# Kernel optimization log

Measured on AMD Instinct MI355X. Metric: run time of the kernel, lower is better.

The kernel has to match this reference:

```python
import jax, jax.numpy as jnp
import numpy as np

N_NODES = 100000
N_EDGES = 1600000
IN_DIM = 128
OUT_DIM = 64


def setup_inputs() -> dict:
    key = jax.random.key(0)
    k1, k2, k3, k4, k5 = jax.random.split(key, 5)
    return {
        "h_init": jax.random.normal(k1, (N_NODES, IN_DIM), dtype=jnp.float32),
        "W1": jax.random.normal(k2, (OUT_DIM, IN_DIM), dtype=jnp.float32),
        "a": jax.random.normal(k3, (1, OUT_DIM), dtype=jnp.float32),
        "src": jax.random.randint(k4, (N_EDGES,), 0, N_NODES, dtype=jnp.int64)
        if jax.config.jax_enable_x64 else jax.random.randint(k4, (N_EDGES,), 0, N_NODES, dtype=jnp.int32),
        "dst": jax.random.randint(k5, (N_EDGES,), 0, N_NODES, dtype=jnp.int32),
    }


def reference(h_init, W1, a, src, dst):
    N = h_init.shape[0]
    # node projection: [N, out_dim]
    h = h_init @ W1.T
    # per-edge diff feature: dst minus src (DGL edges.dst['h'] - edges.src['h'])
    diff = h[dst] - h[src]                       # [E, out_dim]
    e = jnp.tanh(diff @ a[0])                    # [E] edge attention logit
    # segment softmax over incoming edges of each destination node
    seg_max = jax.ops.segment_max(e, dst, num_segments=N)   # [N]
    ex = jnp.exp(e - seg_max[dst])               # [E]
    denom = jax.ops.segment_sum(ex, dst, num_segments=N)    # [N]
    alpha = ex / denom[dst]                      # [E]
    # weighted sum of diff features per destination node
    h_diff = jax.ops.segment_sum(alpha[:, None] * diff, dst, num_segments=N)  # [N, out_dim]
    return jax.nn.relu(h + h_diff)
```

## Files before the change

### kernel.cpp

```cpp
#include <hip/hip_runtime.h>
#include <hip/hip_fp16.h>

#define N_NODES 100000
#define N_EDGES 1600000
#define IN_DIM 128
#define OUT_DIM 64

#define PROJ_BLKS 1563

#define NB2 782
#define MAXB2 2560
#define CUR_STRIDE 16

#define BIN_NBLK 250
#define BIN_CHUNK 6400
#define BIN_THREADS 1024

#define SG_THREADS 512

typedef short short8 __attribute__((ext_vector_type(8)));
typedef float f32x4 __attribute__((ext_vector_type(4)));

__device__ __forceinline__ short bf16_trunc(float x) {
  return (short)(__float_as_uint(x) >> 16);
}
__device__ __forceinline__ float bf16_tof(short s) {
  return __uint_as_float(((unsigned)(unsigned short)s) << 16);
}
__device__ __forceinline__ float edge_ex(float p) {
  float t2 = __expf(2.f * p);
  float th = 1.f - 2.f * __builtin_amdgcn_rcpf(t2 + 1.f);
  return __expf(th);
}

__global__ __launch_bounds__(256) void fat1_kernel(
    const float* __restrict__ h_init, const float* __restrict__ W1,
    const float* __restrict__ a, __half* __restrict__ h16,
    float* __restrict__ ha) {
  __shared__ short whi[16 * 64 * 8];
  __shared__ short wlo[16 * 64 * 8];

  for (int idx = threadIdx.x; idx < 16 * 64; idx += 256) {
    int f = idx >> 6;
    int l = idx & 63;
    int kc = f >> 2, ot = f & 3;
    const float* wsrc =
        W1 + (ot * 16 + (l & 15)) * IN_DIM + kc * 32 + (l >> 4) * 8;
    short hi[8], lo[8];
#pragma unroll
    for (int j = 0; j < 8; j++) {
      float x = wsrc[j];
      short hv = bf16_trunc(x);
      hi[j] = hv;
      lo[j] = bf16_trunc(x - bf16_tof(hv));
    }
    *(short8*)&whi[idx * 8] = *(const short8*)hi;
    *(short8*)&wlo[idx * 8] = *(const short8*)lo;
  }

  int row0 = blockIdx.x * 64;
  int w = threadIdx.x >> 6;
  int l = threadIdx.x & 63;
  int m = l & 15;
  int q = l >> 4;

  int arow = row0 + w * 16 + m;
  if (arow >= N_NODES) arow = N_NODES - 1;
  const float* xsrc = h_init + (size_t)arow * IN_DIM + q * 8;

  short8 ahi[4], alo[4];
#pragma unroll
  for (int kc = 0; kc < 4; kc++) {
    float xv[8];
    *(float4*)&xv[0] = *(const float4*)(xsrc + kc * 32);
    *(float4*)&xv[4] = *(const float4*)(xsrc + kc * 32 + 4);
    short hi[8], lo[8];
#pragma unroll
    for (int j = 0; j < 8; j++) {
      short hv = bf16_trunc(xv[j]);
      hi[j] = hv;
      lo[j] = bf16_trunc(xv[j] - bf16_tof(hv));
    }
    ahi[kc] = *(const short8*)hi;
    alo[kc] = *(const short8*)lo;
  }
  __syncthreads();

  f32x4 acc[4] = {{0.f, 0.f, 0.f, 0.f},
                  {0.f, 0.f, 0.f, 0.f},
                  {0.f, 0.f, 0.f, 0.f},
                  {0.f, 0.f, 0.f, 0.f}};

#pragma unroll
  for (int kc = 0; kc < 4; kc++) {
#pragma unroll
    for (int ot = 0; ot < 4; ot++) {
      int base = (((kc << 2) | ot) * 64 + l) * 8;
      short8 bhi = *(const short8*)&whi[base];
      short8 blo = *(const short8*)&wlo[base];
      acc[ot] = __builtin_amdgcn_mfma_f32_16x16x32_bf16(ahi[kc], bhi, acc[ot],
                                                        0, 0, 0);
      acc[ot] = __builtin_amdgcn_mfma_f32_16x16x32_bf16(ahi[kc], blo, acc[ot],
                                                        0, 0, 0);
      acc[ot] = __builtin_amdgcn_mfma_f32_16x16x32_bf16(alo[kc], bhi, acc[ot],
                                                        0, 0, 0);
    }
  }

  float pa[4] = {0.f, 0.f, 0.f, 0.f};
#pragma unroll
  for (int ot = 0; ot < 4; ot++) {
    float aval = a[ot * 16 + m];
#pragma unroll
    for (int r = 0; r < 4; r++) pa[r] += acc[ot][r] * aval;
  }
  int rowb = row0 + w * 16 + q * 4;
#pragma unroll
  for (int r = 0; r < 4; r++) {
    int row = rowb + r;
    if (row < N_NODES) {
#pragma unroll
      for (int ot = 0; ot < 4; ot++)
        h16[(size_t)row * OUT_DIM + ot * 16 + m] = __float2half(acc[ot][r]);
    }
  }
#pragma unroll
  for (int r = 0; r < 4; r++) {
    pa[r] += __shfl_xor(pa[r], 1);
    pa[r] += __shfl_xor(pa[r], 2);
    pa[r] += __shfl_xor(pa[r], 4);
    pa[r] += __shfl_xor(pa[r], 8);
  }
  if (m == 0) {
#pragma unroll
    for (int r = 0; r < 4; r++) {
      int row = rowb + r;
      if (row < N_NODES) ha[row] = pa[r];
    }
  }
}

__global__ __launch_bounds__(BIN_THREADS) void bin_scatter_kernel(
    const int* __restrict__ src, const int* __restrict__ dst,
    int* __restrict__ bucket_cursor, unsigned int* __restrict__ pairs) {
  __shared__ int hst[NB2];
  __shared__ int cur[NB2];
  __shared__ int dlds[BIN_CHUNK];
  int t = threadIdx.x;
  for (int i = t; i < NB2; i += BIN_THREADS) hst[i] = 0;
  __syncthreads();
  int beg = blockIdx.x * BIN_CHUNK;
  for (int e = t; e < BIN_CHUNK; e += BIN_THREADS) {
    int d = dst[beg + e];
    dlds[e] = d;
    atomicAdd(&hst[d >> 7], 1);
  }
  __syncthreads();
  for (int i = t; i < NB2; i += BIN_THREADS) {
    int c = hst[i];
    cur[i] =
        (c > 0) ? atomicAdd(&bucket_cursor[i * CUR_STRIDE], c) + i * MAXB2 : 0;
  }
  __syncthreads();
  for (int e = t; e < BIN_CHUNK; e += BIN_THREADS) {
    int d = dlds[e];
    int pos = atomicAdd(&cur[d >> 7], 1);
    pairs[pos] = ((unsigned int)src[beg + e] << 7) | (unsigned int)(d & 127);
  }
}

__global__ __launch_bounds__(SG_THREADS) void sortgather_kernel(
    const __half* __restrict__ h16, const float* __restrict__ ha,
    const int* __restrict__ bucket_cursor, const unsigned int* __restrict__
        pairs, float* __restrict__ out) {
  __shared__ unsigned int plds[MAXB2];
  __shared__ int2 slds[MAXB2];
  __shared__ float had[128];
  __shared__ int hist[128];
  __shared__ int scn[128];
  __shared__ int cur[128];
  int b = blockIdx.x;
  int t = threadIdx.x;
  int node0 = b << 7;
  int cnt = min(bucket_cursor[b * CUR_STRIDE], MAXB2);

  if (t < 128) {
    int node = node0 + t;
    had[t] = (node < N_NODES) ? ha[node] : 0.f;
    hist[t] = 0;
  }
  __syncthreads();
  for (int i = t; i < cnt; i += SG_THREADS) {
    unsigned int p = pairs[(size_t)b * MAXB2 + i];
    plds[i] = p;
    atomicAdd(&hist[p & 127u], 1);
  }
  __syncthreads();
  int v = (t < 128) ? hist[t] : 0;
  if (t < 128) scn[t] = v;
  __syncthreads();
  for (int off = 1; off < 128; off <<= 1) {
    int u = (t >= off && t < 128) ? scn[t - off] : 0;
    __syncthreads();
    if (t < 128) scn[t] += u;
    __syncthreads();
  }
  if (t < 128) cur[t] = scn[t] - v;
  __syncthreads();
  for (int i = t; i < cnt; i += SG_THREADS) {
    unsigned int p = plds[i];
    int nl = (int)(p & 127u);
    int sb = (int)(p & 0xFFFFFF80u);
    float ex = edge_ex(had[nl] - ha[sb >> 7]);
    int pos = atomicAdd(&cur[nl], 1);
    slds[pos] = make_int2(sb, __float_as_int(ex));
  }
  __syncthreads();

  int sg = t >> 3;
  int l8 = t & 7;
  const char* h16b = (const char*)h16;
  float4* o4 = (float4*)out;

  for (int nl = sg; nl < 128; nl += 64) {
    int node = node0 + nl;
    if (node >= N_NODES) continue;
    int endp = scn[nl];
    int begp = endp - hist[nl];
    union {
      uint4 u;
      __half hh[8];
    } HD;
    HD.u = *(const uint4*)(h16b + ((size_t)node << 7) + (l8 << 4));
    float acc[8] = {0.f, 0.f, 0.f, 0.f, 0.f, 0.f, 0.f, 0.f};
    float den = 0.f;
    int last = endp - 1;

    for (int base = begp; base < endp; base += 4) {
      int2 e[4];
      float exv[4];
#pragma unroll
      for (int k = 0; k < 4; k++) {
        int i = base + k;
        e[k] = slds[i < endp ? i : last];
        exv[k] = (i < endp) ? __int_as_float(e[k].y) : 0.f;
      }
      uint4 uv[4];
#pragma unroll
      for (int k = 0; k < 4; k++)
        uv[k] = *(const uint4*)(h16b + e[k].x + (l8 << 4));
#pragma unroll
      for (int k = 0; k < 4; k++) {
        union {
          uint4 u;
          __half hh[8];
        } U;
        U.u = uv[k];
        float ex = exv[k];
        den += ex;
#pragma unroll
        for (int j = 0; j < 8; j++)
          acc[j] = fmaf(__half2float(U.hh[j]), ex, acc[j]);
      }
    }

    bool has = den > 0.f;
    float inv = has ? __builtin_amdgcn_rcpf(den) : 0.f;
    float hd[8];
#pragma unroll
    for (int j = 0; j < 8; j++) hd[j] = __half2float(HD.hh[j]);
    float4 r0, r1;
    r0.x = fmaxf(has ? 2.f * hd[0] - acc[0] * inv : hd[0], 0.f);
    r0.y = fmaxf(has ? 2.f * hd[1] - acc[1] * inv : hd[1], 0.f);
    r0.z = fmaxf(has ? 2.f * hd[2] - acc[2] * inv : hd[2], 0.f);
    r0.w = fmaxf(has ? 2.f * hd[3] - acc[3] * inv : hd[3], 0.f);
    r1.x = fmaxf(has ? 2.f * hd[4] - acc[4] * inv : hd[4], 0.f);
    r1.y = fmaxf(has ? 2.f * hd[5] - acc[5] * inv : hd[5], 0.f);
    r1.z = fmaxf(has ? 2.f * hd[6] - acc[6] * inv : hd[6], 0.f);
    r1.w = fmaxf(has ? 2.f * hd[7] - acc[7] * inv : hd[7], 0.f);
    o4[(size_t)node * (OUT_DIM / 4) + l8 * 2] = r0;
    o4[(size_t)node * (OUT_DIM / 4) + l8 * 2 + 1] = r1;
  }
}

extern "C" void kernel_launch(void* const* d_in, const int* in_sizes, int n_in,
                              void* d_out, int out_size, void* d_ws,
                              size_t ws_size, hipStream_t stream) {
  const float* h_init = (const float*)d_in[0];
  const float* W1 = (const float*)d_in[1];
  const float* a = (const float*)d_in[2];
  const int* src = (const int*)d_in[3];
  const int* dst = (const int*)d_in[4];
  float* out = (float*)d_out;

  __half* h16 = (__half*)d_ws;
  float* ha = (float*)(h16 + (size_t)N_NODES * OUT_DIM);
  unsigned int* pairs = (unsigned int*)(ha + N_NODES);
  int* bucket_cursor = (int*)(pairs + (size_t)NB2 * MAXB2);

  hipMemsetAsync(bucket_cursor, 0, NB2 * CUR_STRIDE * sizeof(int), stream);
  fat1_kernel<<<PROJ_BLKS, 256, 0, stream>>>(h_init, W1, a, h16, ha);
  bin_scatter_kernel<<<BIN_NBLK, BIN_THREADS, 0, stream>>>(src, dst,
                                                           bucket_cursor,
                                                           pairs);
  sortgather_kernel<<<NB2, SG_THREADS, 0, stream>>>(h16, ha, bucket_cursor,
                                                    pairs, out);
}
```

Measured before the change: 183.0 us.

## Fuse edge binning into projection kernel and use wave-shuffle prefix scan

Folds the edge bucketing pass into the projection kernel: every fourth projection block, after finishing its rows, bins a 4096-edge chunk using vectorized int4 loads of src/dst, reusing the weight shared memory for the histogram. This removes a separate kernel launch and lets binning overlap with projection work. The sort-gather kernel also loads pairs with uint4 and replaces the multi-barrier LDS Hillis-Steele scan with a wave shuffle scan. The fused blocks run longer, so load is imbalanced, and the binning now rereads dst instead of caching it in LDS.

```diff
diff --git a/kernel.cpp b/kernel.cpp
--- a/kernel.cpp
+++ b/kernel.cpp
@@ -12,9 +12,7 @@
 #define MAXB2 2560
 #define CUR_STRIDE 16
 
-#define BIN_NBLK 250
-#define BIN_CHUNK 6400
-#define BIN_THREADS 1024
+#define BCHUNK 4096
 
 #define SG_THREADS 512
 
@@ -35,12 +33,17 @@
 
 __global__ __launch_bounds__(256) void fat1_kernel(
     const float* __restrict__ h_init, const float* __restrict__ W1,
-    const float* __restrict__ a, __half* __restrict__ h16,
-    float* __restrict__ ha) {
-  __shared__ short whi[16 * 64 * 8];
-  __shared__ short wlo[16 * 64 * 8];
-
-  for (int idx = threadIdx.x; idx < 16 * 64; idx += 256) {
+    const float* __restrict__ a, const int* __restrict__ src,
+    const int* __restrict__ dst, __half* __restrict__ h16,
+    float* __restrict__ ha, int* __restrict__ bucket_cursor,
+    unsigned int* __restrict__ pairs) {
+  __shared__ __align__(16) char smem[16 * 64 * 8 * 2 * sizeof(short)];
+  short* whi = (short*)smem;
+  short* wlo = whi + 16 * 64 * 8;
+  int pb = blockIdx.x;
+  int t = threadIdx.x;
+
+  for (int idx = t; idx < 16 * 64; idx += 256) {
     int f = idx >> 6;
     int l = idx & 63;
     int kc = f >> 2, ot = f & 3;
@@ -58,9 +61,9 @@
     *(short8*)&wlo[idx * 8] = *(const short8*)lo;
   }
 
-  int row0 = blockIdx.x * 64;
-  int w = threadIdx.x >> 6;
-  int l = threadIdx.x & 63;
+  int row0 = pb * 64;
+  int w = t >> 6;
+  int l = t & 63;
   int m = l & 15;
   int q = l >> 4;
 
@@ -138,47 +141,55 @@
       if (row < N_NODES) ha[row] = pa[r];
     }
   }
-}
-
-__global__ __launch_bounds__(BIN_THREADS) void bin_scatter_kernel(
-    const int* __restrict__ src, const int* __restrict__ dst,
-    int* __restrict__ bucket_cursor, unsigned int* __restrict__ pairs) {
-  __shared__ int hst[NB2];
-  __shared__ int cur[NB2];
-  __shared__ int dlds[BIN_CHUNK];
-  int t = threadIdx.x;
-  for (int i = t; i < NB2; i += BIN_THREADS) hst[i] = 0;
-  __syncthreads();
-  int beg = blockIdx.x * BIN_CHUNK;
-  for (int e = t; e < BIN_CHUNK; e += BIN_THREADS) {
-    int d = dst[beg + e];
-    dlds[e] = d;
-    atomicAdd(&hst[d >> 7], 1);
-  }
-  __syncthreads();
-  for (int i = t; i < NB2; i += BIN_THREADS) {
+
+  if ((pb & 3) != 0) return;
+  int cb = pb >> 2;
+  int beg = cb * BCHUNK;
+  int end = min(beg + BCHUNK, N_EDGES);
+
+  __syncthreads();
+  int* hst = (int*)smem;
+  int* cur = hst + NB2;
+  for (int i = t; i < NB2; i += 256) hst[i] = 0;
+  __syncthreads();
+  for (int e = beg + t * 4; e < end; e += 256 * 4) {
+    int4 d4 = *(const int4*)&dst[e];
+    atomicAdd(&hst[d4.x >> 7], 1);
+    atomicAdd(&hst[d4.y >> 7], 1);
+    atomicAdd(&hst[d4.z >> 7], 1);
+    atomicAdd(&hst[d4.w >> 7], 1);
+  }
+  __syncthreads();
+  for (int i = t; i < NB2; i += 256) {
     int c = hst[i];
     cur[i] =
         (c > 0) ? atomicAdd(&bucket_cursor[i * CUR_STRIDE], c) + i * MAXB2 : 0;
   }
   __syncthreads();
-  for (int e = t; e < BIN_CHUNK; e += BIN_THREADS) {
-    int d = dlds[e];
-    int pos = atomicAdd(&cur[d >> 7], 1);
-    pairs[pos] = ((unsigned int)src[beg + e] << 7) | (unsigned int)(d & 127);
+  for (int e = beg + t * 4; e < end; e += 256 * 4) {
+    int4 s4 = *(const int4*)&src[e];
+    int4 d4 = *(const int4*)&dst[e];
+    int ss[4] = {s4.x, s4.y, s4.z, s4.w};
+    int dd[4] = {d4.x, d4.y, d4.z, d4.w};
+#pragma unroll
+    for (int k = 0; k < 4; k++) {
+      int pos = atomicAdd(&cur[dd[k] >> 7], 1);
+      pairs[pos] = ((unsigned)ss[k] << 7) | (unsigned)(dd[k] & 127);
+    }
   }
 }
 
 __global__ __launch_bounds__(SG_THREADS) void sortgather_kernel(
     const __half* __restrict__ h16, const float* __restrict__ ha,
-    const int* __restrict__ bucket_cursor, const unsigned int* __restrict__
-        pairs, float* __restrict__ out) {
+    const int* __restrict__ bucket_cursor,
+    const unsigned int* __restrict__ pairs, float* __restrict__ out) {
   __shared__ unsigned int plds[MAXB2];
   __shared__ int2 slds[MAXB2];
   __shared__ float had[128];
   __shared__ int hist[128];
   __shared__ int scn[128];
   __shared__ int cur[128];
+  __shared__ int wsum;
   int b = blockIdx.x;
   int t = threadIdx.x;
   int node0 = b << 7;
@@ -190,22 +201,35 @@
     hist[t] = 0;
   }
   __syncthreads();
-  for (int i = t; i < cnt; i += SG_THREADS) {
+  int c4 = cnt & ~3;
+  for (int i = t * 4; i < c4; i += SG_THREADS * 4) {
+    uint4 p4 = *(const uint4*)&pairs[(size_t)b * MAXB2 + i];
+    *(uint4*)&plds[i] = p4;
+    atomicAdd(&hist[p4.x & 127u], 1);
+    atomicAdd(&hist[p4.y & 127u], 1);
+    atomicAdd(&hist[p4.z & 127u], 1);
+    atomicAdd(&hist[p4.w & 127u], 1);
+  }
+  for (int i = c4 + t; i < cnt; i += SG_THREADS) {
     unsigned int p = pairs[(size_t)b * MAXB2 + i];
     plds[i] = p;
     atomicAdd(&hist[p & 127u], 1);
   }
   __syncthreads();
   int v = (t < 128) ? hist[t] : 0;
-  if (t < 128) scn[t] = v;
-  __syncthreads();
-  for (int off = 1; off < 128; off <<= 1) {
-    int u = (t >= off && t < 128) ? scn[t - off] : 0;
-    __syncthreads();
-    if (t < 128) scn[t] += u;
-    __syncthreads();
-  }
-  if (t < 128) cur[t] = scn[t] - v;
+  int x = v;
+#pragma unroll
+  for (int off = 1; off < 64; off <<= 1) {
+    int y = __shfl_up(x, off, 64);
+    if ((t & 63) >= off) x += y;
+  }
+  if (t == 63) wsum = x;
+  __syncthreads();
+  if (t >= 64 && t < 128) x += wsum;
+  if (t < 128) {
+    scn[t] = x;
+    cur[t] = x - v;
+  }
   __syncthreads();
   for (int i = t; i < cnt; i += SG_THREADS) {
     unsigned int p = plds[i];
@@ -299,10 +323,8 @@
   int* bucket_cursor = (int*)(pairs + (size_t)NB2 * MAXB2);
 
   hipMemsetAsync(bucket_cursor, 0, NB2 * CUR_STRIDE * sizeof(int), stream);
-  fat1_kernel<<<PROJ_BLKS, 256, 0, stream>>>(h_init, W1, a, h16, ha);
-  bin_scatter_kernel<<<BIN_NBLK, BIN_THREADS, 0, stream>>>(src, dst,
-                                                           bucket_cursor,
-                                                           pairs);
+  fat1_kernel<<<PROJ_BLKS, 256, 0, stream>>>(h_init, W1, a, src, dst, h16, ha,
+                                             bucket_cursor, pairs);
   sortgather_kernel<<<NB2, SG_THREADS, 0, stream>>>(h16, ha, bucket_cursor,
                                                     pairs, out);
 }
```

Result: slower. 202.7 us (+10.8%).
